# Kernel optimization log

Hardware: AMD Instinct MI355X
Metric: run time of the kernel (lower is better)

## Reference

```python
import jax, jax.numpy as jnp
import numpy as np

DIM = 1024
NUM_HEADS = 16
DH = DIM // NUM_HEADS  # 64
B, S = 4, 2048


def setup_inputs() -> dict:
    key = jax.random.key(0)
    ks = jax.random.split(key, 9)
    sc = 0.02
    x = jax.random.normal(ks[0], (B, S, DIM), dtype=jnp.float32)
    # per-head projection weights stacked: [H, DIM, DH] (input-major layout)
    Wq = jax.random.normal(ks[1], (NUM_HEADS, DIM, DH), dtype=jnp.float32) * sc
    Wk = jax.random.normal(ks[2], (NUM_HEADS, DIM, DH), dtype=jnp.float32) * sc
    Wv = jax.random.normal(ks[3], (NUM_HEADS, DIM, DH), dtype=jnp.float32) * sc
    bq = jax.random.normal(ks[4], (NUM_HEADS, DH), dtype=jnp.float32) * sc
    bk = jax.random.normal(ks[5], (NUM_HEADS, DH), dtype=jnp.float32) * sc
    bv = jax.random.normal(ks[6], (NUM_HEADS, DH), dtype=jnp.float32) * sc
    Wo = jax.random.normal(ks[7], (DIM, DIM), dtype=jnp.float32) * sc  # (in, out)
    bo = jax.random.normal(ks[8], (DIM,), dtype=jnp.float32) * sc
    return {"x": x, "Wq": Wq, "Wk": Wk, "Wv": Wv,
            "bq": bq, "bk": bk, "bv": bv, "Wo": Wo, "bo": bo}


def reference(x, Wq, Wk, Wv, bq, bk, bv, Wo, bo):
    # Per-head Linear projections, vectorized over heads: [B,H,S,DH]
    q = jnp.einsum('bsd,hde->bhse', x, Wq) + bq[None, :, None, :]
    k = jnp.einsum('bsd,hde->bhse', x, Wk) + bk[None, :, None, :]
    v = jnp.einsum('bsd,hde->bhse', x, Wv) + bv[None, :, None, :]
    # attention_matmul: Q @ K^T normalized by sqrt(dim_per_head)
    scale = 1.0 / jnp.sqrt(jnp.asarray(DH, dtype=x.dtype))
    scores = jnp.einsum('bhse,bhte->bhst', q, k) * scale  # [B,H,S,S]
    attn = jax.nn.softmax(scores, axis=-1)
    # attn_drop with p=0.0 is identity
    o = jnp.einsum('bhst,bhte->bhse', attn, v)  # [B,H,S,DH]
    # concat along last dim in head order -> [B,S,H*DH]
    o = jnp.transpose(o, (0, 2, 1, 3)).reshape(x.shape[0], x.shape[1], NUM_HEADS * DH)
    # output projection (proj_drop p=0.0 is identity)
    return o @ Wo + bo
```

## Files before the change

kernel.cpp:

```cpp
#include <hip/hip_runtime.h>
#include <stdint.h>

#define DIM 1024
#define NH 16
#define DH 64
#define BATCH 4
#define SEQ 2048
#define MROWS (BATCH*SEQ)

typedef _Float16 half8 __attribute__((ext_vector_type(8)));
typedef __fp16 fp16x2 __attribute__((ext_vector_type(2)));
typedef float f32x4 __attribute__((ext_vector_type(4)));
typedef float f32x16 __attribute__((ext_vector_type(16)));
typedef unsigned int u32x2 __attribute__((ext_vector_type(2)));

__device__ __forceinline__ unsigned short f2h(float f) {
    union { _Float16 h; unsigned short u; } c; c.h = (_Float16)f; return c.u;
}
__device__ __forceinline__ unsigned int pk2u(float a, float b) {
    union { fp16x2 h; unsigned int u; } c;
    c.h = __builtin_amdgcn_cvt_pkrtz(a, b);
    return c.u;
}
__device__ __forceinline__ float fexp2(float x) {
    return __builtin_amdgcn_exp2f(x);
}
__device__ __forceinline__ void gl_lds16(const unsigned short* g, unsigned short* l) {
    __builtin_amdgcn_global_load_lds(
        (__attribute__((address_space(1))) void*)(void*)g,
        (__attribute__((address_space(3))) void*)(void*)l,
        16, 0, 0);
}

__global__ __launch_bounds__(256) void cast_prep_kernel(
    const float* __restrict__ x, unsigned short* __restrict__ xh,
    const float* __restrict__ Wq, const float* __restrict__ Wk,
    const float* __restrict__ Wv, const float* __restrict__ Wo,
    unsigned short* __restrict__ wt, unsigned short* __restrict__ wot)
{
    __shared__ unsigned short tile[64][65];
    const int bid = blockIdx.x;
    if (bid < 8192) {
        const int i = bid * 256 + threadIdx.x;
        float4 v = reinterpret_cast<const float4*>(x)[i];
        uint2 o;
        o.x = pk2u(v.x, v.y);
        o.y = pk2u(v.z, v.w);
        reinterpret_cast<uint2*>(xh)[i] = o;
        return;
    }
    const int local = bid - 8192;
    const int d0 = (local & 15) * 64;
    const int y = (local >> 4) & 15;
    const int mat = local >> 8;
    const int c = threadIdx.x & 63;
    const int rr = threadIdx.x >> 6;

    if (mat < 3) {
        const float* W = (mat == 0) ? Wq : ((mat == 1) ? Wk : Wv);
#pragma unroll
        for (int p = 0; p < 16; p++) {
            int dl = p * 4 + rr;
            tile[dl][c] = f2h(W[((size_t)y * 1024 + d0 + dl) * 64 + c]);
        }
        __syncthreads();
#pragma unroll
        for (int p = 0; p < 16; p++) {
            int el = p * 4 + rr;
            wt[(((size_t)(mat * NH + y) * 64) + el) * DIM + d0 + c] = tile[c][el];
        }
    } else {
        const int o0 = y * 64;
#pragma unroll
        for (int p = 0; p < 16; p++) {
            int dl = p * 4 + rr;
            tile[dl][c] = f2h(Wo[(size_t)(d0 + dl) * DIM + o0 + c]);
        }
        __syncthreads();
#pragma unroll
        for (int p = 0; p < 16; p++) {
            int ol = p * 4 + rr;
            wot[(size_t)(o0 + ol) * DIM + d0 + c] = tile[c][ol];
        }
    }
}

__global__ __launch_bounds__(256) void qkv_gemm_kernel(
    const unsigned short* __restrict__ xh,
    const unsigned short* __restrict__ wt,
    const float* __restrict__ bq, const float* __restrict__ bk,
    const float* __restrict__ bv,
    unsigned short* __restrict__ Qb,
    unsigned short* __restrict__ Kb,
    unsigned short* __restrict__ Vt)
{
    const int bid = blockIdx.x;
    const int xcd = bid & 7;
    const int local = bid >> 3;
    const int rowblk = xcd * 8 + local / 24;
    const int rem = local % 24;
    const int hpair = rem & 7;
    const int mat = rem >> 3;

    const int wave = threadIdx.x >> 6;
    const int lane = threadIdx.x & 63;
    const int ql = lane & 31;
    const int hi = lane >> 5;
    const int mhalf = wave & 1;
    const int nhalf = wave >> 1;

    __shared__ __align__(16) unsigned short pool[16384];
    unsigned short* AbP = pool;
    unsigned short* BtP = pool + 8192;

    const unsigned short* Asrc = xh + (size_t)rowblk * 128 * DIM;
    const unsigned short* Bsrc = wt + (size_t)(mat * NH + hpair * 2) * DH * DIM;

    const int srow = lane >> 2;
    const int scs = lane & 3;

    f32x16 z16;
#pragma unroll
    for (int e = 0; e < 16; e++) z16[e] = 0.f;
    f32x16 acc[2][2];
#pragma unroll
    for (int mt = 0; mt < 2; mt++)
#pragma unroll
        for (int nt = 0; nt < 2; nt++) acc[mt][nt] = z16;

    auto stage = [&](int k0, int sel) {
#pragma unroll
        for (int jj = 0; jj < 2; jj++) {
            const int j = wave * 2 + jj;
            const int r = j * 16 + srow;
            const int cg = scs ^ ((srow >> 1) & 3) ^ ((j * 2 + (srow >> 3)) & 3);
            gl_lds16(Asrc + (size_t)r * DIM + k0 + cg * 8, AbP + sel * 4096 + j * 512);
            gl_lds16(Bsrc + (size_t)r * DIM + k0 + cg * 8, BtP + sel * 4096 + j * 512);
        }
    };

    const int slotx = ((ql >> 1) & 3) ^ ((ql >> 3) & 3);
    int arow[2], brow[2], sks[2];
#pragma unroll
    for (int t = 0; t < 2; t++) {
        arow[t] = (mhalf * 64 + t * 32 + ql) * 32;
        brow[t] = (nhalf * 64 + t * 32 + ql) * 32;
    }
#pragma unroll
    for (int ks = 0; ks < 2; ks++) sks[ks] = ((ks * 2 + hi) ^ slotx) * 8;

    stage(0, 0);
    __syncthreads();

    for (int i = 0; i < DIM / 32; i++) {
        const int sel = i & 1;
        if (i + 1 < DIM / 32) stage((i + 1) * 32, sel ^ 1);

#pragma unroll
        for (int ks = 0; ks < 2; ks++) {
            half8 a0 = *reinterpret_cast<const half8*>(AbP + sel * 4096 + arow[0] + sks[ks]);
            half8 a1 = *reinterpret_cast<const half8*>(AbP + sel * 4096 + arow[1] + sks[ks]);
            half8 b0 = *reinterpret_cast<const half8*>(BtP + sel * 4096 + brow[0] + sks[ks]);
            half8 b1 = *reinterpret_cast<const half8*>(BtP + sel * 4096 + brow[1] + sks[ks]);
            acc[0][0] = __builtin_amdgcn_mfma_f32_32x32x16_f16(a0, b0, acc[0][0], 0, 0, 0);
            acc[0][1] = __builtin_amdgcn_mfma_f32_32x32x16_f16(a0, b1, acc[0][1], 0, 0, 0);
            acc[1][0] = __builtin_amdgcn_mfma_f32_32x32x16_f16(a1, b0, acc[1][0], 0, 0, 0);
            acc[1][1] = __builtin_amdgcn_mfma_f32_32x32x16_f16(a1, b1, acc[1][1], 0, 0, 0);
        }
        __syncthreads();
    }

    const float* bias = (mat == 0) ? bq : ((mat == 1) ? bk : bv);
    const float scale = (mat == 0) ? 0.1803368801111601f : 1.0f;
    const int rowBase = rowblk * 128 + mhalf * 64;
    const int bb = rowBase / SEQ;
    const int sBase = rowBase % SEQ;

    if (mat < 2) {
        unsigned short* outp = (mat == 0) ? Qb : Kb;
#pragma unroll
        for (int mt = 0; mt < 2; mt++) {
#pragma unroll
            for (int nt = 0; nt < 2; nt++) {
                const int e = nhalf * 64 + nt * 32 + ql;
                const int head = hpair * 2 + (e >> 6);
                const int n = e & 63;
                const float bvl = bias[head * DH + n];
                const size_t base = (size_t)(bb * NH + head) * SEQ * DH;
#pragma unroll
                for (int r = 0; r < 16; r++) {
                    const int s = sBase + mt * 32 + (r & 3) + 8 * (r >> 2) + 4 * hi;
                    outp[base + (size_t)s * DH + n] =
                        f2h((acc[mt][nt][r] + bvl) * scale);
                }
            }
        }
    } else {
#pragma unroll
        for (int mt = 0; mt < 2; mt++) {
#pragma unroll
            for (int nt = 0; nt < 2; nt++) {
                const int el = nhalf * 64 + nt * 32 + ql;
                const int head = hpair * 2 + (el >> 6);
                const int n = el & 63;
                const float bvl = bias[head * DH + n];
                const int xsw = (el & 7) << 2;
#pragma unroll
                for (int g = 0; g < 4; g++) {
                    const int slot = mhalf * 16 + mt * 8 + 2 * g + hi;
                    uint2 w;
                    w.x = pk2u(acc[mt][nt][4 * g + 0] + bvl, acc[mt][nt][4 * g + 1] + bvl);
                    w.y = pk2u(acc[mt][nt][4 * g + 2] + bvl, acc[mt][nt][4 * g + 3] + bvl);
                    *reinterpret_cast<uint2*>(pool + el * 128 + (slot ^ xsw) * 4) = w;
                }
            }
        }
        __syncthreads();
        const int blkRow = rowblk * 128;
        const int vb = blkRow / SEQ;
        const int s0b = blkRow % SEQ;
        const int sc = threadIdx.x & 15;
        const int esub = threadIdx.x >> 4;
#pragma unroll
        for (int p = 0; p < 8; p++) {
            const int el = p * 16 + esub;
            const int head = hpair * 2 + (el >> 6);
            const int n = el & 63;
            const int rs = (sc * 2) ^ ((el & 7) << 2);
            uint4 v = *reinterpret_cast<const uint4*>(pool + el * 128 + rs * 4);
            const size_t base = (size_t)(vb * NH + head) * DH * SEQ;
            *reinterpret_cast<uint4*>(&Vt[base + (size_t)n * SEQ + s0b + sc * 8]) = v;
        }
    }
}

__global__ __launch_bounds__(256, 4) void attn_kernel(
    const unsigned short* __restrict__ Qb,
    const unsigned short* __restrict__ Kb,
    const unsigned short* __restrict__ Vt,
    unsigned short* __restrict__ Ob)
{
    const int bid = blockIdx.x;
    const int xcd = bid & 7;
    const int local = bid >> 3;
    const int bhg = xcd * 8 + (local >> 4);
    const int qblk = local & 15;
    const int h = bhg & 15;
    const int bb = bhg >> 4;

    const int wave = threadIdx.x >> 6;
    const int lane = threadIdx.x & 63;
    const int ql = lane & 31;
    const int hi = lane >> 5;
    const int qBase = qblk * 128 + wave * 32;

    const size_t bh = (size_t)(bb * NH + h);
    const unsigned short* Qh = Qb + bh * SEQ * DH;
    const unsigned short* Kh = Kb + bh * SEQ * DH;
    const unsigned short* Vh = Vt + bh * DH * SEQ;

    __shared__ __align__(16) unsigned short Kbuf[2][64 * 64];
    __shared__ __align__(16) unsigned short Vbuf[2][64 * 64];

    const int srow = lane >> 3;
    const int scs = lane & 7;
    int koff[2], voff[2];
#pragma unroll
    for (int jj = 0; jj < 2; jj++) {
        const int r = wave * 16 + jj * 8 + srow;
        const int cg = scs ^ srow ^ ((wave * 2 + jj) & 3);
        koff[jj] = r * DH + cg * 8;
        voff[jj] = r * SEQ + cg * 8;
    }

    auto stage_k = [&](int kt, int sel) {
        const size_t base = (size_t)kt * 64 * DH;
        gl_lds16(Kh + base + koff[0], &Kbuf[sel][wave * 1024]);
        gl_lds16(Kh + base + koff[1], &Kbuf[sel][wave * 1024 + 512]);
    };
    auto stage_v = [&](int kt, int sel) {
        const size_t base = (size_t)kt * 64;
        gl_lds16(Vh + base + voff[0], &Vbuf[sel][wave * 1024]);
        gl_lds16(Vh + base + voff[1], &Vbuf[sel][wave * 1024 + 512]);
    };

    half8 qf[4];
#pragma unroll
    for (int ks = 0; ks < 4; ks++)
        qf[ks] = *reinterpret_cast<const half8*>(
            Qh + (size_t)(qBase + ql) * DH + ks * 16 + hi * 8);

    const int slotx = (ql & 7) ^ ((ql >> 3) & 3);
    int rowb[2], soff[4];
#pragma unroll
    for (int b = 0; b < 2; b++) rowb[b] = (b * 32 + ql) * 64;
#pragma unroll
    for (int ks = 0; ks < 4; ks++) soff[ks] = ((ks * 2 + hi) ^ slotx) * 8;

    f32x16 z16;
#pragma unroll
    for (int e = 0; e < 16; e++) z16[e] = 0.f;

    f32x16 o[2];
#pragma unroll
    for (int mt = 0; mt < 2; mt++) o[mt] = z16;
    float lsA = 0.f, lsB = 0.f;

    auto compute = [&](int sel) {
#pragma unroll
        for (int kb = 0; kb < 2; kb++) {
            f32x16 sacc;
            __builtin_amdgcn_s_setprio(1);
#pragma unroll
            for (int ks = 0; ks < 4; ks++) {
                half8 kf = *reinterpret_cast<const half8*>(
                    &Kbuf[sel][rowb[kb] + soff[ks]]);
                sacc = __builtin_amdgcn_mfma_f32_32x32x16_f16(
                    kf, qf[ks], ks ? sacc : z16, 0, 0, 0);
            }
            __builtin_amdgcn_s_setprio(0);

            unsigned int c[8];
#pragma unroll
            for (int m = 0; m < 8; m++) {
                float a = fexp2(sacc[2 * m]);
                float b2 = fexp2(sacc[2 * m + 1]);
                if (m & 1) lsB += a + b2; else lsA += a + b2;
                c[m] = pk2u(a, b2);
            }

            __builtin_amdgcn_s_setprio(1);
#pragma unroll
            for (int ks = 0; ks < 2; ks++) {
                u32x2 w02 = __builtin_amdgcn_permlane32_swap(
                    c[4 * ks + 0], c[4 * ks + 2], false, false);
                u32x2 w13 = __builtin_amdgcn_permlane32_swap(
                    c[4 * ks + 1], c[4 * ks + 3], false, false);
                union { unsigned int u[4]; half8 h; } cv;
                cv.u[0] = w02[0]; cv.u[1] = w13[0];
                cv.u[2] = w02[1]; cv.u[3] = w13[1];
                const half8 pf = cv.h;
#pragma unroll
                for (int mt = 0; mt < 2; mt++) {
                    half8 vf = *reinterpret_cast<const half8*>(
                        &Vbuf[sel][rowb[mt] + soff[kb * 2 + ks]]);
                    o[mt] = __builtin_amdgcn_mfma_f32_32x32x16_f16(
                        vf, pf, o[mt], 0, 0, 0);
                }
            }
            __builtin_amdgcn_s_setprio(0);
        }
    };

    stage_k(0, 0);
    stage_v(0, 0);
    __syncthreads();

    for (int i = 0; i < SEQ / 64; i++) {
        const int sel = i & 1;
        if (i + 1 < SEQ / 64) {
            stage_k(i + 1, sel ^ 1);
            stage_v(i + 1, sel ^ 1);
        }
        compute(sel);
        __syncthreads();
    }

    float l = lsA + lsB;
    l += __shfl_xor(l, 32);
    const float inv = 1.f / l;
    const size_t orow = (size_t)(bb * SEQ + qBase + ql) * DIM + h * DH;
#pragma unroll
    for (int mt = 0; mt < 2; mt++) {
#pragma unroll
        for (int g = 0; g < 4; g++) {
            uint2 pkd;
            pkd.x = pk2u(o[mt][4 * g + 0] * inv, o[mt][4 * g + 1] * inv);
            pkd.y = pk2u(o[mt][4 * g + 2] * inv, o[mt][4 * g + 3] * inv);
            *reinterpret_cast<uint2*>(Ob + orow + mt * 32 + 8 * g + 4 * hi) = pkd;
        }
    }
}

__global__ __launch_bounds__(256) void out_proj_kernel(
    const unsigned short* __restrict__ Ob,
    const unsigned short* __restrict__ wot,
    const float* __restrict__ bo,
    float* __restrict__ out)
{
    const int bid = blockIdx.x;
    const int xcd = bid & 7;
    const int local = bid >> 3;
    const int rowblk = xcd * 8 + (local >> 3);
    const int colblk = local & 7;

    const int wave = threadIdx.x >> 6;
    const int lane = threadIdx.x & 63;
    const int ql = lane & 31;
    const int hi = lane >> 5;
    const int mhalf = wave & 1;
    const int nhalf = wave >> 1;

    __shared__ __align__(16) unsigned short Ab[2][128 * 32];
    __shared__ __align__(16) unsigned short Bt[2][128 * 32];

    const unsigned short* Asrc = Ob + (size_t)rowblk * 128 * DIM;
    const unsigned short* Bsrc = wot + (size_t)colblk * 128 * DIM;

    const int srow = lane >> 2;
    const int scs = lane & 3;

    f32x16 z16;
#pragma unroll
    for (int e = 0; e < 16; e++) z16[e] = 0.f;
    f32x16 acc[2][2];
#pragma unroll
    for (int mt = 0; mt < 2; mt++)
#pragma unroll
        for (int nt = 0; nt < 2; nt++) acc[mt][nt] = z16;

    auto stage = [&](int k0, int sel) {
#pragma unroll
        for (int jj = 0; jj < 2; jj++) {
            const int j = wave * 2 + jj;
            const int r = j * 16 + srow;
            const int cg = scs ^ ((srow >> 1) & 3) ^ ((j * 2 + (srow >> 3)) & 3);
            gl_lds16(Asrc + (size_t)r * DIM + k0 + cg * 8, &Ab[sel][j * 512]);
            gl_lds16(Bsrc + (size_t)r * DIM + k0 + cg * 8, &Bt[sel][j * 512]);
        }
    };

    const int slotx = ((ql >> 1) & 3) ^ ((ql >> 3) & 3);
    int arow[2], brow[2], sks[2];
#pragma unroll
    for (int t = 0; t < 2; t++) {
        arow[t] = (mhalf * 64 + t * 32 + ql) * 32;
        brow[t] = (nhalf * 64 + t * 32 + ql) * 32;
    }
#pragma unroll
    for (int ks = 0; ks < 2; ks++) sks[ks] = ((ks * 2 + hi) ^ slotx) * 8;

    stage(0, 0);
    __syncthreads();

    for (int i = 0; i < DIM / 32; i++) {
        const int sel = i & 1;
        if (i + 1 < DIM / 32) stage((i + 1) * 32, sel ^ 1);

#pragma unroll
        for (int ks = 0; ks < 2; ks++) {
            half8 a0 = *reinterpret_cast<const half8*>(&Ab[sel][arow[0] + sks[ks]]);
            half8 a1 = *reinterpret_cast<const half8*>(&Ab[sel][arow[1] + sks[ks]]);
            half8 b0 = *reinterpret_cast<const half8*>(&Bt[sel][brow[0] + sks[ks]]);
            half8 b1 = *reinterpret_cast<const half8*>(&Bt[sel][brow[1] + sks[ks]]);
            acc[0][0] = __builtin_amdgcn_mfma_f32_32x32x16_f16(a0, b0, acc[0][0], 0, 0, 0);
            acc[0][1] = __builtin_amdgcn_mfma_f32_32x32x16_f16(a0, b1, acc[0][1], 0, 0, 0);
            acc[1][0] = __builtin_amdgcn_mfma_f32_32x32x16_f16(a1, b0, acc[1][0], 0, 0, 0);
            acc[1][1] = __builtin_amdgcn_mfma_f32_32x32x16_f16(a1, b1, acc[1][1], 0, 0, 0);
        }
        __syncthreads();
    }

    const int rowBase = rowblk * 128 + mhalf * 64;
    const int colBase = colblk * 128 + nhalf * 64;
#pragma unroll
    for (int mt = 0; mt < 2; mt++) {
#pragma unroll
        for (int nt = 0; nt < 2; nt++) {
            const int col = colBase + nt * 32 + ql;
            const float bias = bo[col];
#pragma unroll
            for (int r = 0; r < 16; r++) {
                const int row = rowBase + mt * 32 + (r & 3) + 8 * (r >> 2) + 4 * hi;
                out[(size_t)row * DIM + col] = acc[mt][nt][r] + bias;
            }
        }
    }
}


extern "C" void kernel_launch(void* const* d_in, const int* in_sizes, int n_in,
                              void* d_out, int out_size, void* d_ws, size_t ws_size,
                              hipStream_t stream) {
    const float* x  = (const float*)d_in[0];
    const float* Wq = (const float*)d_in[1];
    const float* Wk = (const float*)d_in[2];
    const float* Wv = (const float*)d_in[3];
    const float* bq = (const float*)d_in[4];
    const float* bk = (const float*)d_in[5];
    const float* bv = (const float*)d_in[6];
    const float* Wo = (const float*)d_in[7];
    const float* bo = (const float*)d_in[8];
    float* out = (float*)d_out;

    unsigned short* xh  = (unsigned short*)d_ws;
    unsigned short* wt  = xh  + (size_t)MROWS * DIM;
    unsigned short* wot = wt  + (size_t)3 * NH * DH * DIM;
    unsigned short* Qb  = wot + (size_t)DIM * DIM;
    unsigned short* Kb  = Qb  + (size_t)BATCH * NH * SEQ * DH;
    unsigned short* Vt  = Kb  + (size_t)BATCH * NH * SEQ * DH;
    unsigned short* Ob  = Vt  + (size_t)BATCH * NH * SEQ * DH;

    cast_prep_kernel<<<9216, 256, 0, stream>>>(x, xh, Wq, Wk, Wv, Wo, wt, wot);
    qkv_gemm_kernel<<<1536, 256, 0, stream>>>(xh, wt, bq, bk, bv, Qb, Kb, Vt);
    attn_kernel<<<1024, 256, 0, stream>>>(Qb, Kb, Vt, Ob);
    out_proj_kernel<<<512, 256, 0, stream>>>(Ob, wot, bo, out);
}
```

Baseline: 284.2 us.

## Use partial vmcnt waits and raw barriers for double-buffered LDS pipelines

Replaces the __syncthreads-based double-buffer loops in the QKV GEMM, attention and output-projection kernels with explicit s_barrier plus s_waitcnt vmcnt(4). This lets the next tile's global-to-LDS loads stay in flight while the current tile is computed, instead of draining all loads at each barrier. Scheduling fences keep the compiler from reordering across these points. The risk is correctness if the vmcnt count does not match the number of outstanding loads, and the added fences may limit instruction interleaving.

```diff
diff --git a/kernel.cpp b/kernel.cpp
--- a/kernel.cpp
+++ b/kernel.cpp
@@ -31,6 +31,10 @@
         (__attribute__((address_space(3))) void*)(void*)l,
         16, 0, 0);
 }
+#define SFENCE __builtin_amdgcn_sched_barrier(0)
+#define SBAR   __builtin_amdgcn_s_barrier()
+#define VMCNT4 asm volatile("s_waitcnt vmcnt(4)" ::: "memory")
+#define VMCNT0 asm volatile("s_waitcnt vmcnt(0)" ::: "memory")
 
 __global__ __launch_bounds__(256) void cast_prep_kernel(
     const float* __restrict__ x, unsigned short* __restrict__ xh,
@@ -149,13 +153,7 @@
 #pragma unroll
     for (int ks = 0; ks < 2; ks++) sks[ks] = ((ks * 2 + hi) ^ slotx) * 8;
 
-    stage(0, 0);
-    __syncthreads();
-
-    for (int i = 0; i < DIM / 32; i++) {
-        const int sel = i & 1;
-        if (i + 1 < DIM / 32) stage((i + 1) * 32, sel ^ 1);
-
+    auto compute = [&](int sel) {
 #pragma unroll
         for (int ks = 0; ks < 2; ks++) {
             half8 a0 = *reinterpret_cast<const half8*>(AbP + sel * 4096 + arow[0] + sks[ks]);
@@ -167,8 +165,21 @@
             acc[1][0] = __builtin_amdgcn_mfma_f32_32x32x16_f16(a1, b0, acc[1][0], 0, 0, 0);
             acc[1][1] = __builtin_amdgcn_mfma_f32_32x32x16_f16(a1, b1, acc[1][1], 0, 0, 0);
         }
-        __syncthreads();
-    }
+    };
+
+    stage(0, 0);
+    for (int i = 0; i < DIM / 32 - 1; i++) {
+        const int sel = i & 1;
+        SFENCE; SBAR; SFENCE;
+        stage((i + 1) * 32, sel ^ 1);
+        SFENCE; VMCNT4; SFENCE;
+        SBAR; SFENCE;
+        compute(sel);
+    }
+    SFENCE; VMCNT0; SFENCE;
+    SBAR; SFENCE;
+    compute((DIM / 32 - 1) & 1);
+    __syncthreads();
 
     const float* bias = (mat == 0) ? bq : ((mat == 1) ? bk : bv);
     const float scale = (mat == 0) ? 0.1803368801111601f : 1.0f;
@@ -253,6 +264,7 @@
     const int ql = lane & 31;
     const int hi = lane >> 5;
     const int qBase = qblk * 128 + wave * 32;
+    const int NT = SEQ / 64;
 
     const size_t bh = (size_t)(bb * NH + h);
     const unsigned short* Qh = Qb + bh * SEQ * DH;
@@ -273,15 +285,13 @@
         voff[jj] = r * SEQ + cg * 8;
     }
 
-    auto stage_k = [&](int kt, int sel) {
-        const size_t base = (size_t)kt * 64 * DH;
-        gl_lds16(Kh + base + koff[0], &Kbuf[sel][wave * 1024]);
-        gl_lds16(Kh + base + koff[1], &Kbuf[sel][wave * 1024 + 512]);
-    };
-    auto stage_v = [&](int kt, int sel) {
-        const size_t base = (size_t)kt * 64;
-        gl_lds16(Vh + base + voff[0], &Vbuf[sel][wave * 1024]);
-        gl_lds16(Vh + base + voff[1], &Vbuf[sel][wave * 1024 + 512]);
+    auto stage_kv = [&](int kt, int sel) {
+        const size_t kb0 = (size_t)kt * 64 * DH;
+        const size_t vb0 = (size_t)kt * 64;
+        gl_lds16(Kh + kb0 + koff[0], &Kbuf[sel][wave * 1024]);
+        gl_lds16(Kh + kb0 + koff[1], &Kbuf[sel][wave * 1024 + 512]);
+        gl_lds16(Vh + vb0 + voff[0], &Vbuf[sel][wave * 1024]);
+        gl_lds16(Vh + vb0 + voff[1], &Vbuf[sel][wave * 1024 + 512]);
     };
 
     half8 qf[4];
@@ -352,19 +362,18 @@
         }
     };
 
-    stage_k(0, 0);
-    stage_v(0, 0);
-    __syncthreads();
-
-    for (int i = 0; i < SEQ / 64; i++) {
+    stage_kv(0, 0);
+    for (int i = 0; i < NT - 1; i++) {
         const int sel = i & 1;
-        if (i + 1 < SEQ / 64) {
-            stage_k(i + 1, sel ^ 1);
-            stage_v(i + 1, sel ^ 1);
-        }
+        SFENCE; SBAR; SFENCE;
+        stage_kv(i + 1, sel ^ 1);
+        SFENCE; VMCNT4; SFENCE;
+        SBAR; SFENCE;
         compute(sel);
-        __syncthreads();
-    }
+    }
+    SFENCE; VMCNT0; SFENCE;
+    SBAR; SFENCE;
+    compute((NT - 1) & 1);
 
     float l = lsA + lsB;
     l += __shfl_xor(l, 32);
@@ -440,13 +449,7 @@
 #pragma unroll
     for (int ks = 0; ks < 2; ks++) sks[ks] = ((ks * 2 + hi) ^ slotx) * 8;
 
-    stage(0, 0);
-    __syncthreads();
-
-    for (int i = 0; i < DIM / 32; i++) {
-        const int sel = i & 1;
-        if (i + 1 < DIM / 32) stage((i + 1) * 32, sel ^ 1);
-
+    auto compute = [&](int sel) {
 #pragma unroll
         for (int ks = 0; ks < 2; ks++) {
             half8 a0 = *reinterpret_cast<const half8*>(&Ab[sel][arow[0] + sks[ks]]);
@@ -458,8 +461,20 @@
             acc[1][0] = __builtin_amdgcn_mfma_f32_32x32x16_f16(a1, b0, acc[1][0], 0, 0, 0);
             acc[1][1] = __builtin_amdgcn_mfma_f32_32x32x16_f16(a1, b1, acc[1][1], 0, 0, 0);
         }
-        __syncthreads();
-    }
+    };
+
+    stage(0, 0);
+    for (int i = 0; i < DIM / 32 - 1; i++) {
+        const int sel = i & 1;
+        SFENCE; SBAR; SFENCE;
+        stage((i + 1) * 32, sel ^ 1);
+        SFENCE; VMCNT4; SFENCE;
+        SBAR; SFENCE;
+        compute(sel);
+    }
+    SFENCE; VMCNT0; SFENCE;
+    SBAR; SFENCE;
+    compute((DIM / 32 - 1) & 1);
 
     const int rowBase = rowblk * 128 + mhalf * 64;
     const int colBase = colblk * 128 + nhalf * 64;
```

New measurement: 300.6 us. 1.06x slower.
